# Kernel tuning notes

Hardware: AMD Instinct MI355X
Metric: run time of the kernel (lower is better)

## Reference

```python
import jax, jax.numpy as jnp
import numpy as np


def setup_inputs() -> dict:
    key = jax.random.key(0)
    k1, k2, k3, k4 = jax.random.split(key, 4)
    Na, Nb, Da, Db, S = 200000, 200000, 64, 64, 256
    a_locations = jax.random.randint(k1, (Na, 3), 0, S, dtype=jnp.int32)
    b_locations = jax.random.randint(k2, (Nb, 3), 0, S, dtype=jnp.int32)
    a_features = jax.random.normal(k3, (Na, Da), dtype=jnp.float32)
    b_features = jax.random.normal(k4, (Nb, Db), dtype=jnp.float32)
    return {
        "a_locations": a_locations,
        "a_features": a_features,
        "b_locations": b_locations,
        "b_features": b_features,
    }


def reference(a_locations, a_features, b_locations, b_features):
    # Stack all locations and dedup rows (torch.unique(dim=0, return_inverse=True)).
    # For jit-compatibility we use size=N (worst case: no duplicates) and pad
    # trailing unused rows with fill_value=-1 (features rows stay zero).
    locations = jnp.concatenate([a_locations, b_locations], axis=0)  # [N, 3]
    N = locations.shape[0]
    unique_locations, reverse_indices = jnp.unique(
        locations, axis=0, size=N, fill_value=-1, return_inverse=True
    )
    reverse_indices = reverse_indices.ravel()  # [N]

    Na, Da = a_features.shape
    Db = b_features.shape[1]
    a_rev = reverse_indices[:Na]
    b_rev = reverse_indices[Na:]

    # Scatter-concat: a goes into columns [:Da], b into columns [Da:].
    unique_features = jnp.zeros((N, Da + Db), dtype=a_features.dtype)
    unique_features = unique_features.at[a_rev, :Da].set(a_features)
    unique_features = unique_features.at[b_rev, Da:].set(b_features)
    return unique_locations, unique_features
```

## Files before the change

kernel.cpp:

```cpp
#include <hip/hip_runtime.h>
#include <hip/hip_bf16.h>

#define NKEYS   (1 << 24)
#define NW      (NKEYS / 32)
#define WPT     4
#define TPB     256
#define WPB     (TPB * WPT)
#define NBLK2   (NW / WPB)
#define MAXN    400000

__device__ unsigned int g_bits[NW];
__device__ unsigned int g_wordPrefix[NW];
__device__ unsigned int g_blockSums[NBLK2];
__device__ int          g_winner_a[MAXN];
__device__ int          g_winner_b[MAXN];

__global__ void k_init(float* out_loc, int N) {
    int i = blockIdx.x * blockDim.x + threadIdx.x;
    if (i < NW / 4) reinterpret_cast<uint4*>(g_bits)[i] = make_uint4(0u, 0u, 0u, 0u);
    if (i < N) { g_winner_a[i] = -1; g_winner_b[i] = -1; }
    if (i < N * 3) out_loc[i] = -1.0f;
}

__global__ void k_mark(const int* __restrict__ a_loc, const int* __restrict__ b_loc,
                       int Na, int N) {
    int i = blockIdx.x * blockDim.x + threadIdx.x;
    if (i >= N) return;
    const int* p = (i < Na) ? (a_loc + (size_t)i * 3) : (b_loc + (size_t)(i - Na) * 3);
    int key = (p[0] << 16) | (p[1] << 8) | p[2];
    atomicOr(&g_bits[key >> 5], 1u << (key & 31));
}

__global__ void k_reduce() {
    __shared__ unsigned int s[TPB];
    int b = blockIdx.x, t = threadIdx.x;
    uint4 w = reinterpret_cast<const uint4*>(g_bits)[b * TPB + t];
    s[t] = __popc(w.x) + __popc(w.y) + __popc(w.z) + __popc(w.w);
    __syncthreads();
    for (int off = TPB / 2; off > 0; off >>= 1) {
        if (t < off) s[t] += s[t + off];
        __syncthreads();
    }
    if (t == 0) g_blockSums[b] = s[0];
}

__global__ void k_scan() {
    __shared__ unsigned int s[NBLK2];
    int t = threadIdx.x;
    unsigned int v = g_blockSums[t];
    s[t] = v;
    __syncthreads();
    for (int off = 1; off < NBLK2; off <<= 1) {
        unsigned int u = (t >= off) ? s[t - off] : 0u;
        __syncthreads();
        s[t] += u;
        __syncthreads();
    }
    g_blockSums[t] = s[t] - v;
}

__global__ void k_prefix_loc(float* __restrict__ out_loc) {
    __shared__ unsigned int s[TPB];
    int b = blockIdx.x, t = threadIdx.x;
    int w0 = (b * TPB + t) * WPT;
    uint4 wv = reinterpret_cast<const uint4*>(g_bits)[b * TPB + t];
    unsigned int wlocal[WPT] = { wv.x, wv.y, wv.z, wv.w };
    unsigned int cnt = __popc(wv.x) + __popc(wv.y) + __popc(wv.z) + __popc(wv.w);
    s[t] = cnt;
    __syncthreads();
    for (int off = 1; off < TPB; off <<= 1) {
        unsigned int u = (t >= off) ? s[t - off] : 0u;
        __syncthreads();
        s[t] += u;
        __syncthreads();
    }
    unsigned int r = g_blockSums[b] + s[t] - cnt;
#pragma unroll
    for (int j = 0; j < WPT; ++j) {
        unsigned int bits = wlocal[j];
        g_wordPrefix[w0 + j] = r;
        while (bits) {
            int bit = __ffs(bits) - 1;
            bits &= bits - 1;
            int key = ((w0 + j) << 5) | bit;
            float* p = out_loc + (size_t)r * 3;
            p[0] = (float)(key >> 16);
            p[1] = (float)((key >> 8) & 255);
            p[2] = (float)(key & 255);
            ++r;
        }
    }
}

__global__ void k_reverse(const int* __restrict__ a_loc, const int* __restrict__ b_loc,
                          int Na, int N) {
    int i = blockIdx.x * blockDim.x + threadIdx.x;
    if (i >= N) return;
    const int* p = (i < Na) ? (a_loc + (size_t)i * 3) : (b_loc + (size_t)(i - Na) * 3);
    int key = (p[0] << 16) | (p[1] << 8) | p[2];
    unsigned int word = g_bits[key >> 5];
    unsigned int r = g_wordPrefix[key >> 5] + __popc(word & ((1u << (key & 31)) - 1u));
    if (i < Na) atomicMax(&g_winner_a[r], i);
    else        atomicMax(&g_winner_b[r], i - Na);
}

__global__ void k_gather(const float* __restrict__ a_feat, const float* __restrict__ b_feat,
                         float* __restrict__ out_feat, int N) {
    int idx = blockIdx.x * blockDim.x + threadIdx.x;
    if (idx >= N * 32) return;
    int u  = idx >> 5;
    int c4 = (idx & 31) * 4;
    float4 v = make_float4(0.f, 0.f, 0.f, 0.f);
    if (c4 < 64) {
        int w = g_winner_a[u];
        if (w >= 0) v = *reinterpret_cast<const float4*>(a_feat + (size_t)w * 64 + c4);
    } else {
        int w = g_winner_b[u];
        if (w >= 0) v = *reinterpret_cast<const float4*>(b_feat + (size_t)w * 64 + (c4 - 64));
    }
    *reinterpret_cast<float4*>(out_feat + (size_t)u * 128 + c4) = v;
}

extern "C" void kernel_launch(void* const* d_in, const int* in_sizes, int n_in,
                              void* d_out, int out_size, void* d_ws, size_t ws_size,
                              hipStream_t stream) {
    const int*   a_loc  = (const int*)  d_in[0];
    const float* a_feat = (const float*)d_in[1];
    const int*   b_loc  = (const int*)  d_in[2];
    const float* b_feat = (const float*)d_in[3];

    const int Na = in_sizes[0] / 3;
    const int Nb = in_sizes[2] / 3;
    const int N  = Na + Nb;

    float* out_loc  = (float*)d_out;
    float* out_feat = out_loc + (size_t)N * 3;

    k_init<<<(N * 3 + TPB - 1) / TPB, TPB, 0, stream>>>(out_loc, N);
    k_mark<<<(N + TPB - 1) / TPB, TPB, 0, stream>>>(a_loc, b_loc, Na, N);
    k_reduce<<<NBLK2, TPB, 0, stream>>>();
    k_scan<<<1, NBLK2, 0, stream>>>();
    k_prefix_loc<<<NBLK2, TPB, 0, stream>>>(out_loc);
    k_reverse<<<(N + TPB - 1) / TPB, TPB, 0, stream>>>(a_loc, b_loc, Na, N);
    k_gather<<<(N * 32 + TPB - 1) / TPB, TPB, 0, stream>>>(a_feat, b_feat, out_feat, N);
}
```

Measured before the change: 153.6 us.

## Fuse three-kernel bitmap scan into single-pass decoupled look-back scan; nontemporal gather

Replaces the reduce, single-block scan and prefix/location-emit kernels with one kernel. It uses dynamic tile IDs and a decoupled look-back over per-tile status words, which removes two launches and the second pass over the 2 MB bitmap. The feature gather now uses nontemporal loads and stores to reduce cache pollution. The cost is a serial look-back chain with spinning between tiles, which can add latency when predecessor tiles resolve slowly.

After: 285.2 us. 85.6% more time.

```diff
diff --git a/kernel.cpp b/kernel.cpp
--- a/kernel.cpp
+++ b/kernel.cpp
@@ -3,23 +3,27 @@
 
 #define NKEYS   (1 << 24)
 #define NW      (NKEYS / 32)
-#define WPT     4
 #define TPB     256
-#define WPB     (TPB * WPT)
-#define NBLK2   (NW / WPB)
+#define SCAN_BLOCKS 512
 #define MAXN    400000
 
-__device__ unsigned int g_bits[NW];
-__device__ unsigned int g_wordPrefix[NW];
-__device__ unsigned int g_blockSums[NBLK2];
-__device__ int          g_winner_a[MAXN];
-__device__ int          g_winner_b[MAXN];
+typedef float  f32x4 __attribute__((ext_vector_type(4)));
+typedef unsigned int u32x4 __attribute__((ext_vector_type(4)));
+
+__device__ unsigned int        g_bits[NW];
+__device__ unsigned int        g_wordPrefix[NW];
+__device__ unsigned long long  g_tileStatus[SCAN_BLOCKS];
+__device__ unsigned int        g_tileCounter;
+__device__ int                 g_winner_a[MAXN];
+__device__ int                 g_winner_b[MAXN];
 
 __global__ void k_init(float* out_loc, int N) {
     int i = blockIdx.x * blockDim.x + threadIdx.x;
-    if (i < NW / 4) reinterpret_cast<uint4*>(g_bits)[i] = make_uint4(0u, 0u, 0u, 0u);
+    if (i < NW / 4) reinterpret_cast<u32x4*>(g_bits)[i] = (u32x4)(0u);
     if (i < N) { g_winner_a[i] = -1; g_winner_b[i] = -1; }
     if (i < N * 3) out_loc[i] = -1.0f;
+    if (i < SCAN_BLOCKS) g_tileStatus[i] = 0ull;
+    if (i == 0) g_tileCounter = 0u;
 }
 
 __global__ void k_mark(const int* __restrict__ a_loc, const int* __restrict__ b_loc,
@@ -31,40 +35,17 @@
     atomicOr(&g_bits[key >> 5], 1u << (key & 31));
 }
 
-__global__ void k_reduce() {
+__global__ void k_scan_fused(float* __restrict__ out_loc) {
     __shared__ unsigned int s[TPB];
-    int b = blockIdx.x, t = threadIdx.x;
-    uint4 w = reinterpret_cast<const uint4*>(g_bits)[b * TPB + t];
-    s[t] = __popc(w.x) + __popc(w.y) + __popc(w.z) + __popc(w.w);
+    __shared__ unsigned int sTile;
+    __shared__ unsigned int sPrefix;
+    int t = threadIdx.x;
+    if (t == 0) sTile = atomicAdd(&g_tileCounter, 1u);
     __syncthreads();
-    for (int off = TPB / 2; off > 0; off >>= 1) {
-        if (t < off) s[t] += s[t + off];
-        __syncthreads();
-    }
-    if (t == 0) g_blockSums[b] = s[0];
-}
+    unsigned int tile = sTile;
 
-__global__ void k_scan() {
-    __shared__ unsigned int s[NBLK2];
-    int t = threadIdx.x;
-    unsigned int v = g_blockSums[t];
-    s[t] = v;
-    __syncthreads();
-    for (int off = 1; off < NBLK2; off <<= 1) {
-        unsigned int u = (t >= off) ? s[t - off] : 0u;
-        __syncthreads();
-        s[t] += u;
-        __syncthreads();
-    }
-    g_blockSums[t] = s[t] - v;
-}
-
-__global__ void k_prefix_loc(float* __restrict__ out_loc) {
-    __shared__ unsigned int s[TPB];
-    int b = blockIdx.x, t = threadIdx.x;
-    int w0 = (b * TPB + t) * WPT;
-    uint4 wv = reinterpret_cast<const uint4*>(g_bits)[b * TPB + t];
-    unsigned int wlocal[WPT] = { wv.x, wv.y, wv.z, wv.w };
+    u32x4 wv = reinterpret_cast<const u32x4*>(g_bits)[tile * TPB + t];
+    unsigned int wlocal[4] = { wv.x, wv.y, wv.z, wv.w };
     unsigned int cnt = __popc(wv.x) + __popc(wv.y) + __popc(wv.z) + __popc(wv.w);
     s[t] = cnt;
     __syncthreads();
@@ -74,9 +55,35 @@
         s[t] += u;
         __syncthreads();
     }
-    unsigned int r = g_blockSums[b] + s[t] - cnt;
+    unsigned int total = s[TPB - 1];
+
+    if (t == 0) {
+        unsigned long long pkt = ((unsigned long long)((tile == 0) ? 2u : 1u) << 32) | total;
+        __hip_atomic_store(&g_tileStatus[tile], pkt, __ATOMIC_RELEASE, __HIP_MEMORY_SCOPE_AGENT);
+        unsigned int excl = 0u;
+        if (tile > 0) {
+            int p = (int)tile - 1;
+            while (true) {
+                unsigned long long v = __hip_atomic_load(&g_tileStatus[p], __ATOMIC_ACQUIRE,
+                                                         __HIP_MEMORY_SCOPE_AGENT);
+                unsigned int st = (unsigned int)(v >> 32);
+                if (st == 0u) { __builtin_amdgcn_s_sleep(1); continue; }
+                excl += (unsigned int)v;
+                if (st == 2u) break;
+                --p;
+            }
+            __hip_atomic_store(&g_tileStatus[tile],
+                               ((unsigned long long)2u << 32) | (excl + total),
+                               __ATOMIC_RELEASE, __HIP_MEMORY_SCOPE_AGENT);
+        }
+        sPrefix = excl;
+    }
+    __syncthreads();
+
+    unsigned int r = sPrefix + s[t] - cnt;
+    int w0 = (int)(tile * TPB + t) * 4;
 #pragma unroll
-    for (int j = 0; j < WPT; ++j) {
+    for (int j = 0; j < 4; ++j) {
         unsigned int bits = wlocal[j];
         g_wordPrefix[w0 + j] = r;
         while (bits) {
@@ -110,15 +117,17 @@
     if (idx >= N * 32) return;
     int u  = idx >> 5;
     int c4 = (idx & 31) * 4;
-    float4 v = make_float4(0.f, 0.f, 0.f, 0.f);
+    f32x4 v = (f32x4)(0.f);
     if (c4 < 64) {
         int w = g_winner_a[u];
-        if (w >= 0) v = *reinterpret_cast<const float4*>(a_feat + (size_t)w * 64 + c4);
+        if (w >= 0) v = __builtin_nontemporal_load(
+                            reinterpret_cast<const f32x4*>(a_feat + (size_t)w * 64 + c4));
     } else {
         int w = g_winner_b[u];
-        if (w >= 0) v = *reinterpret_cast<const float4*>(b_feat + (size_t)w * 64 + (c4 - 64));
+        if (w >= 0) v = __builtin_nontemporal_load(
+                            reinterpret_cast<const f32x4*>(b_feat + (size_t)w * 64 + (c4 - 64)));
     }
-    *reinterpret_cast<float4*>(out_feat + (size_t)u * 128 + c4) = v;
+    __builtin_nontemporal_store(v, reinterpret_cast<f32x4*>(out_feat + (size_t)u * 128 + c4));
 }
 
 extern "C" void kernel_launch(void* const* d_in, const int* in_sizes, int n_in,
@@ -138,9 +147,7 @@
 
     k_init<<<(N * 3 + TPB - 1) / TPB, TPB, 0, stream>>>(out_loc, N);
     k_mark<<<(N + TPB - 1) / TPB, TPB, 0, stream>>>(a_loc, b_loc, Na, N);
-    k_reduce<<<NBLK2, TPB, 0, stream>>>();
-    k_scan<<<1, NBLK2, 0, stream>>>();
-    k_prefix_loc<<<NBLK2, TPB, 0, stream>>>(out_loc);
+    k_scan_fused<<<SCAN_BLOCKS, TPB, 0, stream>>>(out_loc);
     k_reverse<<<(N + TPB - 1) / TPB, TPB, 0, stream>>>(a_loc, b_loc, Na, N);
     k_gather<<<(N * 32 + TPB - 1) / TPB, TPB, 0, stream>>>(a_feat, b_feat, out_feat, N);
 }
```
